# Kernel optimization log

Hardware: AMD Instinct MI355X
Metric: run time of the kernel (lower is better)

The kernel has to match this reference:

```python
import jax, jax.numpy as jnp
import numpy as np

N, F_IN, H, F_OUT, E = 100000, 128, 4, 8, 1600000


def setup_inputs() -> dict:
    key = jax.random.key(0)
    k1, k2, k3, k4, k5 = jax.random.split(key, 5)
    # Xavier-ish scales
    w_scale = (6.0 / (F_IN + H * F_OUT)) ** 0.5
    a_scale = (6.0 / (1 + F_OUT)) ** 0.5
    return {
        "h_in": jax.random.normal(k1, (N, F_IN), dtype=jnp.float32),
        "W": jax.random.uniform(k2, (H * F_OUT, F_IN), dtype=jnp.float32, minval=-w_scale, maxval=w_scale),
        "b": jnp.zeros((H * F_OUT,), dtype=jnp.float32),
        "a_src": jax.random.uniform(k3, (1, H, F_OUT), dtype=jnp.float32, minval=-a_scale, maxval=a_scale),
        "a_tgt": jax.random.uniform(k4, (1, H, F_OUT), dtype=jnp.float32, minval=-a_scale, maxval=a_scale),
        "edge_index": jax.random.randint(k5, (2, E), 0, N, dtype=jnp.int32),
    }


def reference(h_in, W, b, a_src, a_tgt, edge_index):
    # Dropout treated as identity (eval mode) for a deterministic reference.
    n = h_in.shape[0]
    h_proj = (h_in @ W.T + b).reshape(n, H, F_OUT)  # [N,H,F']
    s_src = jnp.sum(h_proj * a_src, axis=-1)  # [N,H]
    s_tgt = jnp.sum(h_proj * a_tgt, axis=-1)  # [N,H]
    src, tgt = edge_index[0], edge_index[1]
    # per-edge unnormalized attention scores, LeakyReLU(0.2)
    e = jax.nn.leaky_relu(s_src[src] + s_tgt[tgt], negative_slope=0.2)  # [E,H]
    exp_e = jnp.exp(e)  # original code exponentiates without max subtraction
    denom = jax.ops.segment_sum(exp_e, src, num_segments=n)  # [N,H]
    alpha = exp_e / (denom[src] + 1e-16)  # [E,H]
    contrib = alpha[:, :, None] * h_proj[src]  # [E,H,F']
    h_new = jax.ops.segment_sum(contrib, src, num_segments=n)  # [N,H,F']
    # concat=True branch: original returns the raw (un-activated) concat view
    return h_new.reshape(n, H * F_OUT)
```

## Files before the change

### kernel.cpp

```cpp
#include <hip/hip_runtime.h>
#include <hip/hip_bf16.h>

typedef __bf16 bf16x8 __attribute__((ext_vector_type(8)));
typedef float f32x4 __attribute__((ext_vector_type(4)));

#define F_IN 128
#define HF 32
#define LBM_WORDS 4096

__device__ inline bf16x8 cvt8(float4 a, float4 b) {
    bf16x8 r;
    r[0] = (__bf16)a.x; r[1] = (__bf16)a.y; r[2] = (__bf16)a.z; r[3] = (__bf16)a.w;
    r[4] = (__bf16)b.x; r[5] = (__bf16)b.y; r[6] = (__bf16)b.z; r[7] = (__bf16)b.w;
    return r;
}

__global__ __launch_bounds__(256) void mask_build_kernel(
    const int* __restrict__ src, int E,
    unsigned int* __restrict__ bm, int nwords) {
    __shared__ unsigned int lbm[LBM_WORDS];
    const int tid = threadIdx.x;
    const int gtid = blockIdx.x * blockDim.x + tid;
    const int gstride = gridDim.x * blockDim.x;

    if (nwords <= LBM_WORDS) {
        for (int i = tid; i < nwords; i += blockDim.x) lbm[i] = 0u;
        __syncthreads();

        const int nvec = E >> 2;
        const int4* src4 = (const int4*)src;
        for (int i = gtid; i < nvec; i += gstride) {
            int4 v = src4[i];
            atomicOr(&lbm[((unsigned)v.x) >> 5], 1u << (v.x & 31));
            atomicOr(&lbm[((unsigned)v.y) >> 5], 1u << (v.y & 31));
            atomicOr(&lbm[((unsigned)v.z) >> 5], 1u << (v.z & 31));
            atomicOr(&lbm[((unsigned)v.w) >> 5], 1u << (v.w & 31));
        }
        for (int i = (nvec << 2) + gtid; i < E; i += gstride) {
            int s = src[i];
            atomicOr(&lbm[((unsigned)s) >> 5], 1u << (s & 31));
        }
        __syncthreads();

        for (int i = tid; i < nwords; i += blockDim.x) {
            unsigned int w = lbm[i];
            if (w) atomicOr(&bm[i], w);
        }
    } else {
        for (int i = gtid; i < E; i += gstride) {
            int s = src[i];
            atomicOr(&bm[((unsigned)s) >> 5], 1u << (s & 31));
        }
    }
}

__global__ __launch_bounds__(256) void gat_gemm_kernel(
    const float* __restrict__ h_in, const float* __restrict__ W,
    const float* __restrict__ b, const unsigned int* __restrict__ bm,
    float* __restrict__ out, int N) {
    const int tid  = threadIdx.x;
    const int lane = tid & 63;
    const int wave = tid >> 6;
    const int q = lane >> 4;
    const int c = lane & 15;

    const int node_base = blockIdx.x * 128 + wave * 32;
    if (node_base >= N) return;

    bf16x8 bfrag[2][4];
#pragma unroll
    for (int nt = 0; nt < 2; ++nt) {
        const float* wp = W + (nt * 16 + c) * F_IN + q * 8;
#pragma unroll
        for (int ks = 0; ks < 4; ++ks) {
            float4 f0 = *(const float4*)(wp + ks * 32);
            float4 f1 = *(const float4*)(wp + ks * 32 + 4);
            bfrag[nt][ks] = cvt8(f0, f1);
        }
    }

    bf16x8 afrag[2][4];
#pragma unroll
    for (int mt = 0; mt < 2; ++mt) {
        int row = node_base + mt * 16 + c;
        if (row > N - 1) row = N - 1;
        const float* hp = h_in + (long)row * F_IN + q * 8;
#pragma unroll
        for (int ks = 0; ks < 4; ++ks) {
            float4 f0 = *(const float4*)(hp + ks * 32);
            float4 f1 = *(const float4*)(hp + ks * 32 + 4);
            afrag[mt][ks] = cvt8(f0, f1);
        }
    }

    f32x4 acc[2][2] = {{{0.f, 0.f, 0.f, 0.f}, {0.f, 0.f, 0.f, 0.f}},
                       {{0.f, 0.f, 0.f, 0.f}, {0.f, 0.f, 0.f, 0.f}}};
#pragma unroll
    for (int ks = 0; ks < 4; ++ks)
#pragma unroll
        for (int mt = 0; mt < 2; ++mt)
#pragma unroll
            for (int nt = 0; nt < 2; ++nt)
                acc[mt][nt] = __builtin_amdgcn_mfma_f32_16x16x32_bf16(
                    afrag[mt][ks], bfrag[nt][ks], acc[mt][nt], 0, 0, 0);

    const float bias0 = b[c];
    const float bias1 = b[c + 16];

    const unsigned int mword = bm[node_base >> 5];

#pragma unroll
    for (int mt = 0; mt < 2; ++mt) {
        int rowb = node_base + mt * 16 + q * 4;
#pragma unroll
        for (int r = 0; r < 4; ++r) {
            int row = rowb + r;
            if (row < N) {
                float s = ((mword >> (mt * 16 + q * 4 + r)) & 1u) ? 1.0f : 0.0f;
                out[(long)row * HF + c]      = (acc[mt][0][r] + bias0) * s;
                out[(long)row * HF + 16 + c] = (acc[mt][1][r] + bias1) * s;
            }
        }
    }
}

extern "C" void kernel_launch(void* const* d_in, const int* in_sizes, int n_in,
                              void* d_out, int out_size, void* d_ws, size_t ws_size,
                              hipStream_t stream) {
    const float* h_in = (const float*)d_in[0];
    const float* W    = (const float*)d_in[1];
    const float* b    = (const float*)d_in[2];
    const int* edge_index = (const int*)d_in[5];

    const int N = in_sizes[0] / F_IN;
    const int E = in_sizes[5] / 2;

    unsigned int* bm = (unsigned int*)d_ws;
    const int nwords = (N + 31) / 32;

    hipMemsetAsync(bm, 0, (size_t)nwords * sizeof(unsigned int), stream);

    mask_build_kernel<<<128, 256, 0, stream>>>(edge_index, E, bm, nwords);

    int gb = (N + 127) / 128;
    gat_gemm_kernel<<<gb, 256, 0, stream>>>(h_in, W, b, bm,
                                            (float*)d_out, N);
}
```

Measured before the change: 117.0 us.

## Replace global atomic mask merge with per-block partial bitmaps reduced in GEMM

The mask kernel now writes one full partial bitmap per block instead of merging into a shared global bitmap with atomics, and the memset is removed. The GEMM kernel reads the 128 partial words for its 32-node group (two per lane) and OR-reduces them with wave shuffles. This removes the memset launch and the global atomics, at the cost of 128x more bitmap writes and strided partial reads in the GEMM. nwords is 3125, so the single-chunk path is the one that runs.

Result: faster. 114.3 us (-2.3%).

```diff
diff --git a/kernel.cpp b/kernel.cpp
--- a/kernel.cpp
+++ b/kernel.cpp
@@ -7,57 +7,68 @@
 #define F_IN 128
 #define HF 32
 #define LBM_WORDS 4096
+#define MASK_BLOCKS 128
 
-__device__ inline bf16x8 cvt8(float4 a, float4 b) {
-    bf16x8 r;
-    r[0] = (__bf16)a.x; r[1] = (__bf16)a.y; r[2] = (__bf16)a.z; r[3] = (__bf16)a.w;
-    r[4] = (__bf16)b.x; r[5] = (__bf16)b.y; r[6] = (__bf16)b.z; r[7] = (__bf16)b.w;
-    return r;
-}
-
-__global__ __launch_bounds__(256) void mask_build_kernel(
+__global__ __launch_bounds__(256) void mask_partial_kernel(
     const int* __restrict__ src, int E,
-    unsigned int* __restrict__ bm, int nwords) {
+    unsigned int* __restrict__ pbm, int pstride, int nwords) {
     __shared__ unsigned int lbm[LBM_WORDS];
     const int tid = threadIdx.x;
-    const int gtid = blockIdx.x * blockDim.x + tid;
-    const int gstride = gridDim.x * blockDim.x;
+    unsigned int* dst = pbm + (long)blockIdx.x * pstride;
 
-    if (nwords <= LBM_WORDS) {
-        for (int i = tid; i < nwords; i += blockDim.x) lbm[i] = 0u;
+    const int gtid = blockIdx.x * 256 + tid;
+    const int gstride = gridDim.x * 256;
+    const int nvec = E >> 2;
+    const int4* src4 = (const int4*)src;
+
+    for (int cbase = 0; cbase < nwords; cbase += LBM_WORDS) {
+        const int cwords = min(nwords - cbase, LBM_WORDS);
+        for (int i = tid; i < cwords; i += 256) lbm[i] = 0u;
         __syncthreads();
 
-        const int nvec = E >> 2;
-        const int4* src4 = (const int4*)src;
-        for (int i = gtid; i < nvec; i += gstride) {
-            int4 v = src4[i];
-            atomicOr(&lbm[((unsigned)v.x) >> 5], 1u << (v.x & 31));
-            atomicOr(&lbm[((unsigned)v.y) >> 5], 1u << (v.y & 31));
-            atomicOr(&lbm[((unsigned)v.z) >> 5], 1u << (v.z & 31));
-            atomicOr(&lbm[((unsigned)v.w) >> 5], 1u << (v.w & 31));
-        }
-        for (int i = (nvec << 2) + gtid; i < E; i += gstride) {
-            int s = src[i];
-            atomicOr(&lbm[((unsigned)s) >> 5], 1u << (s & 31));
+        if (nwords <= LBM_WORDS) {
+            for (int i = gtid; i < nvec; i += gstride) {
+                int4 v = src4[i];
+                atomicOr(&lbm[((unsigned)v.x) >> 5], 1u << (v.x & 31));
+                atomicOr(&lbm[((unsigned)v.y) >> 5], 1u << (v.y & 31));
+                atomicOr(&lbm[((unsigned)v.z) >> 5], 1u << (v.z & 31));
+                atomicOr(&lbm[((unsigned)v.w) >> 5], 1u << (v.w & 31));
+            }
+            for (int i = (nvec << 2) + gtid; i < E; i += gstride) {
+                int s = src[i];
+                atomicOr(&lbm[((unsigned)s) >> 5], 1u << (s & 31));
+            }
+        } else {
+            const unsigned int lo = (unsigned)cbase << 5;
+            const unsigned int hi = lo + ((unsigned)cwords << 5);
+            for (int i = gtid; i < nvec; i += gstride) {
+                int4 v = src4[i];
+                if ((unsigned)v.x >= lo && (unsigned)v.x < hi)
+                    atomicOr(&lbm[(((unsigned)v.x) >> 5) - cbase], 1u << (v.x & 31));
+                if ((unsigned)v.y >= lo && (unsigned)v.y < hi)
+                    atomicOr(&lbm[(((unsigned)v.y) >> 5) - cbase], 1u << (v.y & 31));
+                if ((unsigned)v.z >= lo && (unsigned)v.z < hi)
+                    atomicOr(&lbm[(((unsigned)v.z) >> 5) - cbase], 1u << (v.z & 31));
+                if ((unsigned)v.w >= lo && (unsigned)v.w < hi)
+                    atomicOr(&lbm[(((unsigned)v.w) >> 5) - cbase], 1u << (v.w & 31));
+            }
+            for (int i = (nvec << 2) + gtid; i < E; i += gstride) {
+                unsigned int s = (unsigned)src[i];
+                if (s >= lo && s < hi)
+                    atomicOr(&lbm[(s >> 5) - cbase], 1u << (s & 31));
+            }
         }
         __syncthreads();
 
-        for (int i = tid; i < nwords; i += blockDim.x) {
-            unsigned int w = lbm[i];
-            if (w) atomicOr(&bm[i], w);
-        }
-    } else {
-        for (int i = gtid; i < E; i += gstride) {
-            int s = src[i];
-            atomicOr(&bm[((unsigned)s) >> 5], 1u << (s & 31));
-        }
+        for (int i = tid; i < cwords; i += 256) dst[cbase + i] = lbm[i];
+        __syncthreads();
     }
 }
 
 __global__ __launch_bounds__(256) void gat_gemm_kernel(
     const float* __restrict__ h_in, const float* __restrict__ W,
-    const float* __restrict__ b, const unsigned int* __restrict__ bm,
-    float* __restrict__ out, int N) {
+    const float* __restrict__ b, const unsigned int* __restrict__ pbm,
+    int pstride, float* __restrict__ out, int N) {
     const int tid  = threadIdx.x;
     const int lane = tid & 63;
     const int wave = tid >> 6;
@@ -66,18 +77,10 @@
 
     const int node_base = blockIdx.x * 128 + wave * 32;
     if (node_base >= N) return;
+    const int wi = node_base >> 5;
 
-    bf16x8 bfrag[2][4];
-#pragma unroll
-    for (int nt = 0; nt < 2; ++nt) {
-        const float* wp = W + (nt * 16 + c) * F_IN + q * 8;
-#pragma unroll
-        for (int ks = 0; ks < 4; ++ks) {
-            float4 f0 = *(const float4*)(wp + ks * 32);
-            float4 f1 = *(const float4*)(wp + ks * 32 + 4);
-            bfrag[nt][ks] = cvt8(f0, f1);
-        }
-    }
+    const unsigned int pm0 = pbm[(long)lane * pstride + wi];
+    const unsigned int pm1 = pbm[(long)(lane + 64) * pstride + wi];
 
     bf16x8 afrag[2][4];
 #pragma unroll
@@ -89,7 +92,25 @@
         for (int ks = 0; ks < 4; ++ks) {
             float4 f0 = *(const float4*)(hp + ks * 32);
             float4 f1 = *(const float4*)(hp + ks * 32 + 4);
-            afrag[mt][ks] = cvt8(f0, f1);
+            bf16x8 r;
+            r[0] = (__bf16)f0.x; r[1] = (__bf16)f0.y; r[2] = (__bf16)f0.z; r[3] = (__bf16)f0.w;
+            r[4] = (__bf16)f1.x; r[5] = (__bf16)f1.y; r[6] = (__bf16)f1.z; r[7] = (__bf16)f1.w;
+            afrag[mt][ks] = r;
+        }
+    }
+
+    bf16x8 bfrag[2][4];
+#pragma unroll
+    for (int nt = 0; nt < 2; ++nt) {
+        const float* wp = W + (nt * 16 + c) * F_IN + q * 8;
+#pragma unroll
+        for (int ks = 0; ks < 4; ++ks) {
+            float4 f0 = *(const float4*)(wp + ks * 32);
+            float4 f1 = *(const float4*)(wp + ks * 32 + 4);
+            bf16x8 r;
+            r[0] = (__bf16)f0.x; r[1] = (__bf16)f0.y; r[2] = (__bf16)f0.z; r[3] = (__bf16)f0.w;
+            r[4] = (__bf16)f1.x; r[5] = (__bf16)f1.y; r[6] = (__bf16)f1.z; r[7] = (__bf16)f1.w;
+            bfrag[nt][ks] = r;
         }
     }
 
@@ -104,10 +125,13 @@
                 acc[mt][nt] = __builtin_amdgcn_mfma_f32_16x16x32_bf16(
                     afrag[mt][ks], bfrag[nt][ks], acc[mt][nt], 0, 0, 0);
 
+    unsigned int mw = pm0 | pm1;
+#pragma unroll
+    for (int off = 32; off; off >>= 1)
+        mw |= (unsigned int)__shfl_xor((int)mw, off);
+
     const float bias0 = b[c];
     const float bias1 = b[c + 16];
-
-    const unsigned int mword = bm[node_base >> 5];
 
 #pragma unroll
     for (int mt = 0; mt < 2; ++mt) {
@@ -116,7 +140,7 @@
         for (int r = 0; r < 4; ++r) {
             int row = rowb + r;
             if (row < N) {
-                float s = ((mword >> (mt * 16 + q * 4 + r)) & 1u) ? 1.0f : 0.0f;
+                float s = ((mw >> (mt * 16 + q * 4 + r)) & 1u) ? 1.0f : 0.0f;
                 out[(long)row * HF + c]      = (acc[mt][0][r] + bias0) * s;
                 out[(long)row * HF + 16 + c] = (acc[mt][1][r] + bias1) * s;
             }
@@ -135,14 +159,14 @@
     const int N = in_sizes[0] / F_IN;
     const int E = in_sizes[5] / 2;
 
-    unsigned int* bm = (unsigned int*)d_ws;
     const int nwords = (N + 31) / 32;
+    const int pstride = (nwords + 63) & ~63;
+    unsigned int* pbm = (unsigned int*)d_ws;
 
-    hipMemsetAsync(bm, 0, (size_t)nwords * sizeof(unsigned int), stream);
-
-    mask_build_kernel<<<128, 256, 0, stream>>>(edge_index, E, bm, nwords);
+    mask_partial_kernel<<<MASK_BLOCKS, 256, 0, stream>>>(
+        edge_index, E, pbm, pstride, nwords);
 
     int gb = (N + 127) / 128;
-    gat_gemm_kernel<<<gb, 256, 0, stream>>>(h_in, W, b, bm,
+    gat_gemm_kernel<<<gb, 256, 0, stream>>>(h_in, W, b, pbm, pstride,
                                             (float*)d_out, N);
 }
```
